# Performance work log

Hardware: AMD Instinct MI355X
Metric: run time of the kernel (lower is better)

## Reference

```python
import jax, jax.numpy as jnp
import numpy as np

NUM_HEADS = 32
NUM_KV_HEADS = 8
HEAD_DIM = 128
GROUPS = NUM_HEADS // NUM_KV_HEADS  # 4
ROPE_BASE = 1000000.0


def _rope_cos_sin(seq_len, dtype):
    inv_freq = 1.0 / (ROPE_BASE ** (jnp.arange(0, HEAD_DIM, 2, dtype=jnp.float32) / HEAD_DIM))
    t = jnp.arange(seq_len, dtype=jnp.float32)
    freqs = jnp.einsum('i,j->ij', t, inv_freq)          # [S, D/2]
    emb = jnp.concatenate([freqs, freqs], axis=-1)       # [S, D]
    return jnp.cos(emb).astype(dtype), jnp.sin(emb).astype(dtype)


def _rotate_half(x):
    x1, x2 = jnp.split(x, 2, axis=-1)
    return jnp.concatenate([-x2, x1], axis=-1)


def setup_inputs() -> dict:
    key = jax.random.key(0)
    k1, k2, k3 = jax.random.split(key, 3)
    B, S, H = 1, 2048, 4096
    hidden_states = jax.random.normal(k1, (B, S, H), dtype=jnp.float32)
    wqkv = jax.random.normal(k2, (6144, H), dtype=jnp.float32) * (H ** -0.5)
    wo = jax.random.normal(k3, (H, H), dtype=jnp.float32) * (H ** -0.5)
    # causal additive mask [B, 1, S, S]
    neg = jnp.finfo(jnp.float32).min
    causal = jnp.triu(jnp.full((S, S), neg, dtype=jnp.float32), k=1)
    attention_mask = causal[None, None]
    position_ids = jnp.broadcast_to(jnp.arange(S, dtype=jnp.int64 if jax.config.jax_enable_x64 else jnp.int32), (B, S))
    return {'hidden_states': hidden_states, 'wqkv': wqkv, 'wo': wo,
            'attention_mask': attention_mask, 'position_ids': position_ids}


def reference(hidden_states, wqkv, wo, attention_mask, position_ids):
    B, S, _ = hidden_states.shape
    qkv = hidden_states @ wqkv.T                               # [B, S, 6144]
    qkv = qkv.reshape(B, S, NUM_KV_HEADS, GROUPS + 2, HEAD_DIM)
    q = qkv[..., :GROUPS, :].reshape(B, S, NUM_HEADS, HEAD_DIM)
    k = qkv[..., -2, :]                                        # [B, S, KVH, D]
    v = qkv[..., -1, :]
    q = q.transpose(0, 2, 1, 3)                                # [B, H, S, D]
    k = k.transpose(0, 2, 1, 3)                                # [B, KVH, S, D]
    v = v.transpose(0, 2, 1, 3)

    cos, sin = _rope_cos_sin(S, hidden_states.dtype)
    cos = cos[position_ids][:, None]                           # [B, 1, S, D]
    sin = sin[position_ids][:, None]
    q = q * cos + _rotate_half(q) * sin
    k = k * cos + _rotate_half(k) * sin

    # repeat_kv: [B, KVH, S, D] -> [B, H, S, D]
    k = jnp.repeat(k, GROUPS, axis=1)
    v = jnp.repeat(v, GROUPS, axis=1)

    scale = 1.0 / jnp.sqrt(jnp.asarray(HEAD_DIM, dtype=q.dtype))
    scores = jnp.einsum('bhqd,bhkd->bhqk', q, k) * scale + attention_mask
    probs = jax.nn.softmax(scores.astype(jnp.float32), axis=-1).astype(q.dtype)
    attn = jnp.einsum('bhqk,bhkd->bhqd', probs, v)             # [B, H, S, D]
    attn = attn.transpose(0, 2, 1, 3).reshape(B, S, NUM_HEADS * HEAD_DIM)
    return attn @ wo.T
```

## Files before the change

kernel.cpp:

```cpp
#include <hip/hip_runtime.h>
#include <stdint.h>

typedef unsigned short u16;
typedef unsigned int u32;
typedef short s16x8 __attribute__((ext_vector_type(8)));
typedef __bf16 bfv8 __attribute__((ext_vector_type(8)));
typedef float f32x4 __attribute__((ext_vector_type(4)));

#define S_LEN 2048
#define HID 4096
#define NQKV 6144

#define MFMA16(d, a, b) (d) = __builtin_amdgcn_mfma_f32_16x16x32_bf16((a), (b), (d), 0, 0, 0)

__device__ __forceinline__ u16 f2bf(float f){
  u32 u = __float_as_uint(f);
  return (u16)((u + 0x7fffu + ((u >> 16) & 1u)) >> 16);
}
__device__ __forceinline__ float bf2f(u16 x){
  return __uint_as_float((u32)x << 16);
}

__global__ __launch_bounds__(256) void cvt_bf16(const float* __restrict__ in,
                                                u16* __restrict__ out, int n4){
  int i = blockIdx.x * 256 + threadIdx.x;
  if (i >= n4) return;
  float4 v = ((const float4*)in)[i];
  ushort4 o;
  o.x = f2bf(v.x); o.y = f2bf(v.y); o.z = f2bf(v.z); o.w = f2bf(v.w);
  ((ushort4*)out)[i] = o;
}

template<typename OT>
__global__ __launch_bounds__(256) void gemm_bt(const u16* __restrict__ A,
                                               const u16* __restrict__ B,
                                               OT* __restrict__ C, int N, int K){
  __shared__ __align__(16) u16 As[128*32];
  __shared__ __align__(16) u16 Bs[128*32];
  const int tid = threadIdx.x;
  const int lane = tid & 63, wave = tid >> 6;
  const int g = lane >> 4, l16 = lane & 15;
  const int wr = wave >> 1, wc = wave & 1;
  const u16* Ag = A + (size_t)blockIdx.y * 128 * K;
  const u16* Bg = B + (size_t)blockIdx.x * 128 * K;
  const int sr0 = (wave*2 + 0)*16 + (lane >> 2);
  const int sr1 = (wave*2 + 1)*16 + (lane >> 2);
  const int su  = lane & 3;
  f32x4 acc[4][4] = {};

#define G_LOAD(k0, ra0, ra1, rb0, rb1)                                    \
  ra0 = *(const s16x8*)(Ag + (size_t)sr0*K + (k0) + su*8);                \
  ra1 = *(const s16x8*)(Ag + (size_t)sr1*K + (k0) + su*8);                \
  rb0 = *(const s16x8*)(Bg + (size_t)sr0*K + (k0) + su*8);                \
  rb1 = *(const s16x8*)(Bg + (size_t)sr1*K + (k0) + su*8);

#define L_STORE(ra0, ra1, rb0, rb1)                                       \
  *(s16x8*)&As[sr0*32 + (su ^ (sr0 & 3))*8] = ra0;                        \
  *(s16x8*)&As[sr1*32 + (su ^ (sr1 & 3))*8] = ra1;                        \
  *(s16x8*)&Bs[sr0*32 + (su ^ (sr0 & 3))*8] = rb0;                        \
  *(s16x8*)&Bs[sr1*32 + (su ^ (sr1 & 3))*8] = rb1;

  {
    s16x8 a0,a1,b0,b1;
    G_LOAD(0, a0,a1,b0,b1)
    L_STORE(a0,a1,b0,b1)
  }
  __syncthreads();
  const int KIT = K >> 5;
  for (int it = 0; it < KIT; it++){
    s16x8 na0,na1,nb0,nb1;
    if (it + 1 < KIT){ G_LOAD((it+1)*32, na0,na1,nb0,nb1) }
    bfv8 af[4], bfr[4];
    #pragma unroll
    for (int i = 0; i < 4; i++){
      int row = wr*64 + i*16 + l16;
      af[i] = *(const bfv8*)&As[row*32 + (g ^ (row & 3))*8];
    }
    #pragma unroll
    for (int j = 0; j < 4; j++){
      int row = wc*64 + j*16 + l16;
      bfr[j] = *(const bfv8*)&Bs[row*32 + (g ^ (row & 3))*8];
    }
    #pragma unroll
    for (int i = 0; i < 4; i++)
      #pragma unroll
      for (int j = 0; j < 4; j++)
        MFMA16(acc[i][j], af[i], bfr[j]);
    __syncthreads();
    if (it + 1 < KIT){ L_STORE(na0,na1,nb0,nb1) }
    __syncthreads();
  }
#undef G_LOAD
#undef L_STORE
  OT* Cp = C + (size_t)(blockIdx.y*128 + wr*64) * N + blockIdx.x*128 + wc*64;
  #pragma unroll
  for (int i = 0; i < 4; i++)
    #pragma unroll
    for (int j = 0; j < 4; j++)
      #pragma unroll
      for (int r = 0; r < 4; r++){
        float v = acc[i][j][r];
        if constexpr (sizeof(OT) == 2)
          Cp[(size_t)(i*16 + g*4 + r) * N + j*16 + l16] = f2bf(v);
        else
          Cp[(size_t)(i*16 + g*4 + r) * N + j*16 + l16] = v;
      }
}

__global__ __launch_bounds__(256) void rope_reorg(const u16* __restrict__ qkv,
                                                  const int* __restrict__ pos,
                                                  u16* __restrict__ Qb, u16* __restrict__ Kb){
  const int hh = blockIdx.x;
  const int s  = blockIdx.y*4 + (threadIdx.x >> 6);
  const int j  = threadIdx.x & 63;
  const float p = (float)pos[s];
  const float inv = __expf(-(float)j * (13.815510557964274f / 64.0f));
  float sn, cs;
  sincosf(p * inv, &sn, &cs);
  const u16* src;
  u16* dst;
  if (hh < 32){
    src = qkv + (size_t)s*NQKV + (hh >> 2)*768 + (hh & 3)*128;
    dst = Qb + ((size_t)hh*S_LEN + s)*128;
  } else {
    int h = hh - 32;
    src = qkv + (size_t)s*NQKV + h*768 + 512;
    dst = Kb + ((size_t)h*S_LEN + s)*128;
  }
  float x1 = bf2f(src[j]), x2 = bf2f(src[j + 64]);
  dst[j]      = f2bf(x1*cs - x2*sn);
  dst[j + 64] = f2bf(x2*cs + x1*sn);
}

__global__ __launch_bounds__(256) void v_transpose(const u16* __restrict__ qkv,
                                                   u16* __restrict__ Vt){
  __shared__ u16 T[64][72];
  const int st = blockIdx.x, dt = blockIdx.y, h = blockIdx.z;
  const int w = threadIdx.x >> 6, lane = threadIdx.x & 63;
  const int s0 = st*64, d0 = dt*64;
  #pragma unroll
  for (int i = 0; i < 16; i++){
    int sl = w*16 + i;
    T[sl][lane] = qkv[(size_t)(s0+sl)*NQKV + h*768 + 640 + d0 + lane];
  }
  __syncthreads();
  #pragma unroll
  for (int i = 0; i < 16; i++){
    int dl = w*16 + i;
    Vt[((size_t)h*128 + d0 + dl)*S_LEN + s0 + lane] = T[lane][dl];
  }
}

__global__ __launch_bounds__(256) void attn_fwd(const u16* __restrict__ Q,
                                                const u16* __restrict__ K,
                                                const u16* __restrict__ V,
                                                u16* __restrict__ O){
  __shared__ __align__(16) u16 Ks[64*128];
  __shared__ __align__(16) u16 Vs[128*64];
  __shared__ __align__(16) u16 Ps[4][16][72];
  const int qblk = blockIdx.x, hq = blockIdx.y, hk = hq >> 2;
  const int tid = threadIdx.x, lane = tid & 63, w = tid >> 6;
  const int g = lane >> 4, l16 = lane & 15;
  const int q0 = qblk*64 + w*16;
  const u16* Qg = Q + ((size_t)hq*S_LEN + q0 + l16)*128;
  bfv8 qf[4];
  #pragma unroll
  for (int kk = 0; kk < 4; kk++) qf[kk] = *(const bfv8*)(Qg + kk*32 + g*8);
  const u16* Kg = K + (size_t)hk*S_LEN*128;
  const u16* Vg = V + (size_t)hk*128*S_LEN;
  f32x4 oacc[8] = {};
  float m_run[4], l_run[4];
  #pragma unroll
  for (int r = 0; r < 4; r++){ m_run[r] = -1e30f; l_run[r] = 0.0f; }
  const float scale = 0.08838834764831845f;

  const int rowk = w*16 + (lane >> 4);
  const int rowv = w*32 + (lane >> 3);

#define KV_LOAD(t, kr, vr)                                                        \
  _Pragma("unroll")                                                               \
  for (int i = 0; i < 4; i++){                                                    \
    kr[i] = *(const s16x8*)(Kg + ((size_t)((t)*64 + rowk + i*4))*128 + (lane & 15)*8); \
    vr[i] = *(const s16x8*)(Vg + (size_t)(rowv + i*8)*S_LEN + (t)*64 + (lane & 7)*8);  \
  }
#define KV_STORE(kr, vr)                                                          \
  _Pragma("unroll")                                                               \
  for (int i = 0; i < 4; i++){                                                    \
    int rk = rowk + i*4, rv = rowv + i*8;                                         \
    *(s16x8*)&Ks[rk*128 + ((lane & 15) ^ (rk & 7))*8] = kr[i];                    \
    *(s16x8*)&Vs[rv*64  + ((lane & 7)  ^ (rv & 7))*8] = vr[i];                    \
  }

  {
    s16x8 kr[4], vr[4];
    KV_LOAD(0, kr, vr)
    KV_STORE(kr, vr)
  }
  __syncthreads();

  for (int t = 0; t <= qblk; t++){
    s16x8 nkr[4], nvr[4];
    if (t + 1 <= qblk){ KV_LOAD(t+1, nkr, nvr) }
    f32x4 sacc[4] = {};
    #pragma unroll
    for (int j = 0; j < 4; j++){
      int row = j*16 + l16;
      #pragma unroll
      for (int kk = 0; kk < 4; kk++){
        bfv8 kf = *(const bfv8*)&Ks[row*128 + ((kk*4 + g) ^ (row & 7))*8];
        MFMA16(sacc[j], qf[kk], kf);
      }
    }
    float sc[4][4];
    #pragma unroll
    for (int j = 0; j < 4; j++)
      #pragma unroll
      for (int r = 0; r < 4; r++)
        sc[j][r] = sacc[j][r] * scale;
    if (t == qblk){
      #pragma unroll
      for (int j = 0; j < 4; j++){
        int kvc = t*64 + j*16 + l16;
        #pragma unroll
        for (int r = 0; r < 4; r++)
          if (kvc > q0 + g*4 + r) sc[j][r] = -1e30f;
      }
    }
    float mx[4];
    #pragma unroll
    for (int r = 0; r < 4; r++)
      mx[r] = fmaxf(fmaxf(sc[0][r], sc[1][r]), fmaxf(sc[2][r], sc[3][r]));
    #pragma unroll
    for (int off = 1; off < 16; off <<= 1)
      #pragma unroll
      for (int r = 0; r < 4; r++)
        mx[r] = fmaxf(mx[r], __shfl_xor(mx[r], off));
    float sf[4], pr[4][4], rsum[4];
    #pragma unroll
    for (int r = 0; r < 4; r++){
      float mn = fmaxf(m_run[r], mx[r]);
      sf[r] = __expf(m_run[r] - mn);
      m_run[r] = mn;
    }
    #pragma unroll
    for (int j = 0; j < 4; j++)
      #pragma unroll
      for (int r = 0; r < 4; r++)
        pr[j][r] = __expf(sc[j][r] - m_run[r]);
    #pragma unroll
    for (int r = 0; r < 4; r++)
      rsum[r] = (pr[0][r] + pr[1][r]) + (pr[2][r] + pr[3][r]);
    #pragma unroll
    for (int off = 1; off < 16; off <<= 1)
      #pragma unroll
      for (int r = 0; r < 4; r++)
        rsum[r] += __shfl_xor(rsum[r], off);
    #pragma unroll
    for (int r = 0; r < 4; r++)
      l_run[r] = l_run[r]*sf[r] + rsum[r];
    #pragma unroll
    for (int n = 0; n < 8; n++)
      #pragma unroll
      for (int r = 0; r < 4; r++)
        oacc[n][r] *= sf[r];
    #pragma unroll
    for (int j = 0; j < 4; j++)
      #pragma unroll
      for (int r = 0; r < 4; r++)
        Ps[w][g*4 + r][j*16 + l16] = f2bf(pr[j][r]);
    bfv8 pf[2];
    #pragma unroll
    for (int kk = 0; kk < 2; kk++)
      pf[kk] = *(const bfv8*)&Ps[w][l16][kk*32 + g*8];
    #pragma unroll
    for (int n = 0; n < 8; n++){
      int drow = n*16 + l16;
      #pragma unroll
      for (int kk = 0; kk < 2; kk++){
        bfv8 vf = *(const bfv8*)&Vs[drow*64 + ((kk*4 + g) ^ (drow & 7))*8];
        MFMA16(oacc[n], pf[kk], vf);
      }
    }
    __syncthreads();
    if (t + 1 <= qblk){ KV_STORE(nkr, nvr) }
    __syncthreads();
  }
#undef KV_LOAD
#undef KV_STORE
  #pragma unroll
  for (int r = 0; r < 4; r++){
    float invl = 1.0f / l_run[r];
    #pragma unroll
    for (int n = 0; n < 8; n++)
      O[(size_t)(q0 + g*4 + r)*HID + hq*128 + n*16 + l16] = f2bf(oacc[n][r]*invl);
  }
}

extern "C" void kernel_launch(void* const* d_in, const int* in_sizes, int n_in,
                              void* d_out, int out_size, void* d_ws, size_t ws_size,
                              hipStream_t stream){
  const float* hidden = (const float*)d_in[0];
  const float* wqkv   = (const float*)d_in[1];
  const float* wo     = (const float*)d_in[2];
  const int*   pos    = (const int*)d_in[4];
  float* out = (float*)d_out;
  char* ws = (char*)d_ws;

  u16* hB    = (u16*)(ws);
  u16* wqkvB = (u16*)(ws + (16ull<<20));
  u16* woB   = (u16*)(ws + (16ull<<20));
  u16* qkvB  = (u16*)(ws + (64ull<<20));
  u16* attnB = (u16*)(ws + (64ull<<20));
  u16* Qb    = (u16*)(ws + (88ull<<20));
  u16* Kb    = (u16*)(ws + (104ull<<20));
  u16* Vtb   = (u16*)(ws + (108ull<<20));

  cvt_bf16<<<dim3(8192),  256, 0, stream>>>(hidden, hB, 2097152);
  cvt_bf16<<<dim3(24576), 256, 0, stream>>>(wqkv, wqkvB, 6291456);
  gemm_bt<u16><<<dim3(48,16), 256, 0, stream>>>(hB, wqkvB, qkvB, NQKV, HID);
  cvt_bf16<<<dim3(16384), 256, 0, stream>>>(wo, woB, 4194304);
  rope_reorg<<<dim3(40,512), 256, 0, stream>>>(qkvB, pos, Qb, Kb);
  v_transpose<<<dim3(32,2,8), 256, 0, stream>>>(qkvB, Vtb);
  attn_fwd<<<dim3(32,32), 256, 0, stream>>>(Qb, Kb, Vtb, attnB);
  gemm_bt<float><<<dim3(32,16), 256, 0, stream>>>(attnB, woB, out, HID, HID);
}
```

Measured before the change: 621.3 us.

## Use direct global-to-LDS double-buffered loads in GEMM and reorder attention grid

The GEMM now loads tiles with global_load_lds straight into double-buffered shared memory. This drops the register staging and one barrier per k-step, and removes the XOR swizzle, which may add LDS bank conflicts on fragment reads. The attention kernel swaps grid axes and reverses the query-block order so the heavier causal blocks are scheduled first, for better load balance.

```diff
diff --git a/kernel.cpp b/kernel.cpp
--- a/kernel.cpp
+++ b/kernel.cpp
@@ -19,6 +19,12 @@
 }
 __device__ __forceinline__ float bf2f(u16 x){
   return __uint_as_float((u32)x << 16);
+}
+
+__device__ __forceinline__ void gl16(const u16* g, u16* l){
+  __builtin_amdgcn_global_load_lds((const __attribute__((address_space(1))) u32*)g,
+                                   (__attribute__((address_space(3))) u32*)l,
+                                   16, 0, 0);
 }
 
 __global__ __launch_bounds__(256) void cvt_bf16(const float* __restrict__ in,
@@ -35,63 +41,48 @@
 __global__ __launch_bounds__(256) void gemm_bt(const u16* __restrict__ A,
                                                const u16* __restrict__ B,
                                                OT* __restrict__ C, int N, int K){
-  __shared__ __align__(16) u16 As[128*32];
-  __shared__ __align__(16) u16 Bs[128*32];
+  __shared__ __align__(16) u16 As[2][128*32];
+  __shared__ __align__(16) u16 Bs[2][128*32];
   const int tid = threadIdx.x;
   const int lane = tid & 63, wave = tid >> 6;
   const int g = lane >> 4, l16 = lane & 15;
   const int wr = wave >> 1, wc = wave & 1;
   const u16* Ag = A + (size_t)blockIdx.y * 128 * K;
   const u16* Bg = B + (size_t)blockIdx.x * 128 * K;
-  const int sr0 = (wave*2 + 0)*16 + (lane >> 2);
-  const int sr1 = (wave*2 + 1)*16 + (lane >> 2);
-  const int su  = lane & 3;
+  const int r0 = wave*32 + (lane >> 2);
+  const int r1 = r0 + 16;
+  const int su = lane & 3;
+  const int l0 = wave*1024;
+  const int l1 = wave*1024 + 512;
   f32x4 acc[4][4] = {};
 
-#define G_LOAD(k0, ra0, ra1, rb0, rb1)                                    \
-  ra0 = *(const s16x8*)(Ag + (size_t)sr0*K + (k0) + su*8);                \
-  ra1 = *(const s16x8*)(Ag + (size_t)sr1*K + (k0) + su*8);                \
-  rb0 = *(const s16x8*)(Bg + (size_t)sr0*K + (k0) + su*8);                \
-  rb1 = *(const s16x8*)(Bg + (size_t)sr1*K + (k0) + su*8);
-
-#define L_STORE(ra0, ra1, rb0, rb1)                                       \
-  *(s16x8*)&As[sr0*32 + (su ^ (sr0 & 3))*8] = ra0;                        \
-  *(s16x8*)&As[sr1*32 + (su ^ (sr1 & 3))*8] = ra1;                        \
-  *(s16x8*)&Bs[sr0*32 + (su ^ (sr0 & 3))*8] = rb0;                        \
-  *(s16x8*)&Bs[sr1*32 + (su ^ (sr1 & 3))*8] = rb1;
-
-  {
-    s16x8 a0,a1,b0,b1;
-    G_LOAD(0, a0,a1,b0,b1)
-    L_STORE(a0,a1,b0,b1)
-  }
+#define ISSUE(b, k0)                                          \
+  gl16(Ag + (size_t)r0*K + (k0) + su*8, &As[b][l0]);          \
+  gl16(Ag + (size_t)r1*K + (k0) + su*8, &As[b][l1]);          \
+  gl16(Bg + (size_t)r0*K + (k0) + su*8, &Bs[b][l0]);          \
+  gl16(Bg + (size_t)r1*K + (k0) + su*8, &Bs[b][l1]);
+
+  ISSUE(0, 0)
   __syncthreads();
   const int KIT = K >> 5;
   for (int it = 0; it < KIT; it++){
-    s16x8 na0,na1,nb0,nb1;
-    if (it + 1 < KIT){ G_LOAD((it+1)*32, na0,na1,nb0,nb1) }
+    const int b = it & 1;
+    if (it + 1 < KIT){ ISSUE(b^1, (it+1)*32) }
     bfv8 af[4], bfr[4];
     #pragma unroll
-    for (int i = 0; i < 4; i++){
-      int row = wr*64 + i*16 + l16;
-      af[i] = *(const bfv8*)&As[row*32 + (g ^ (row & 3))*8];
-    }
-    #pragma unroll
-    for (int j = 0; j < 4; j++){
-      int row = wc*64 + j*16 + l16;
-      bfr[j] = *(const bfv8*)&Bs[row*32 + (g ^ (row & 3))*8];
-    }
+    for (int i = 0; i < 4; i++)
+      af[i] = *(const bfv8*)&As[b][(wr*64 + i*16 + l16)*32 + g*8];
+    #pragma unroll
+    for (int j = 0; j < 4; j++)
+      bfr[j] = *(const bfv8*)&Bs[b][(wc*64 + j*16 + l16)*32 + g*8];
     #pragma unroll
     for (int i = 0; i < 4; i++)
       #pragma unroll
       for (int j = 0; j < 4; j++)
         MFMA16(acc[i][j], af[i], bfr[j]);
     __syncthreads();
-    if (it + 1 < KIT){ L_STORE(na0,na1,nb0,nb1) }
-    __syncthreads();
-  }
-#undef G_LOAD
-#undef L_STORE
+  }
+#undef ISSUE
   OT* Cp = C + (size_t)(blockIdx.y*128 + wr*64) * N + blockIdx.x*128 + wc*64;
   #pragma unroll
   for (int i = 0; i < 4; i++)
@@ -158,7 +149,9 @@
   __shared__ __align__(16) u16 Ks[64*128];
   __shared__ __align__(16) u16 Vs[128*64];
   __shared__ __align__(16) u16 Ps[4][16][72];
-  const int qblk = blockIdx.x, hq = blockIdx.y, hk = hq >> 2;
+  const int hq = blockIdx.x;
+  const int qblk = 31 - blockIdx.y;
+  const int hk = hq >> 2;
   const int tid = threadIdx.x, lane = tid & 63, w = tid >> 6;
   const int g = lane >> 4, l16 = lane & 15;
   const int q0 = qblk*64 + w*16;
```

New measurement: 542.0 us. 1.15x faster.
